# Kernel optimization log

Measured on AMD Instinct MI355X. Metric: run time of the kernel, lower is better.

The kernel has to match this reference:

```python
import jax, jax.numpy as jnp
import numpy as np


def _iterative_inv(mat, n_iter=6):
    # Newton-Schulz iteration for pseudo-inverse of [B,H,M,M] matrices
    I = jnp.eye(mat.shape[-1], dtype=mat.dtype)
    K = mat
    scale = 1.0 / jnp.max(jnp.sum(K, axis=-2), axis=-1)[..., None, None]
    V = scale * jnp.swapaxes(K, -1, -2)
    for _ in range(n_iter):
        KV = K @ V
        V = 0.25 * V @ (13.0 * I - KV @ (15.0 * I - KV @ (7.0 * I - KV)))
    return V


def setup_inputs() -> dict:
    key = jax.random.key(0)
    B, L, d_model, H, M = 4, 4096, 1024, 16, 128
    ks = jax.random.split(key, 11)
    s = 0.02
    return {
        "queries": jax.random.normal(ks[0], (B, L, d_model), jnp.float32),
        "keys": jax.random.normal(ks[1], (B, L, d_model), jnp.float32),
        "values": jax.random.normal(ks[2], (B, L, d_model), jnp.float32),
        "Wq": jax.random.normal(ks[3], (d_model, d_model), jnp.float32) * s,
        "bq": jnp.zeros((d_model,), jnp.float32),
        "Wk": jax.random.normal(ks[4], (d_model, d_model), jnp.float32) * s,
        "bk": jnp.zeros((d_model,), jnp.float32),
        "Wv": jax.random.normal(ks[5], (d_model, d_model), jnp.float32) * s,
        "bv": jnp.zeros((d_model,), jnp.float32),
        "Wo": jax.random.normal(ks[6], (d_model, d_model), jnp.float32) * s,
        "bo": jnp.zeros((d_model,), jnp.float32),
        "n_heads": 16,
        "n_landmarks": 128,
    }


def reference(queries, keys, values, Wq, bq, Wk, bk, Wv, bv, Wo, bo, n_heads, n_landmarks):
    B, L, _ = queries.shape
    H, M = n_heads, n_landmarks
    # projections -> [B, H, L, D]
    q = (queries @ Wq + bq).reshape(B, L, H, -1).transpose(0, 2, 1, 3)
    k = (keys @ Wk + bk).reshape(B, L, H, -1).transpose(0, 2, 1, 3)
    v = (values @ Wv + bv).reshape(B, L, H, -1).transpose(0, 2, 1, 3)
    D = q.shape[-1]
    # landmark pooling: mean over segments of length L//M
    Q_l = q.reshape(B, H, M, L // M, D).mean(axis=-2)
    K_l = k.reshape(B, H, M, L // M, D).mean(axis=-2)
    # three softmax kernels (NOTE: original has no 1/sqrt(D) scaling)
    kernel_1 = jax.nn.softmax(jnp.einsum('bhld,bhmd->bhlm', q, K_l), axis=-1)
    kernel_2 = jax.nn.softmax(jnp.einsum('bhnd,bhmd->bhnm', Q_l, K_l), axis=-1)
    kernel_3 = jax.nn.softmax(jnp.einsum('bhmd,bhld->bhml', Q_l, k), axis=-1)
    # [B,H,L,M] @ [B,H,M,M] @ ([B,H,M,L] @ [B,H,L,D])
    X = kernel_1 @ _iterative_inv(kernel_2) @ (kernel_3 @ v)
    X = X.transpose(0, 2, 1, 3).reshape(B, L, H * D)
    return X @ Wo + bo
```

## Files before the change

### kernel.cpp

```cpp
#include <hip/hip_runtime.h>

typedef __attribute__((ext_vector_type(8))) short s8v;
typedef __attribute__((ext_vector_type(4))) short s4v;
typedef __attribute__((ext_vector_type(4))) float f4v;

#define DEVI static __device__ __forceinline__

DEVI unsigned short f2bf(float f) {
  unsigned u = __float_as_uint(f);
  u = (u + 0x7FFFu + ((u >> 16) & 1u)) >> 16;
  return (unsigned short)u;
}
DEVI float bf2f(unsigned short b) { return __uint_as_float(((unsigned)b) << 16); }

#define MFMA(a, b, c) __builtin_amdgcn_mfma_f32_16x16x32_bf16((a), (b), (c), 0, 0, 0)

__global__ __launch_bounds__(256) void k_wt(const float* __restrict__ W,
                                            unsigned short* __restrict__ WT) {
  __shared__ unsigned short T[64][72];
  const int n0 = blockIdx.x * 64, k0 = blockIdx.y * 64;
  const int t = threadIdx.x;
  {
    const int r = t >> 2, c0 = (t & 3) * 16;
    const float* src = W + (k0 + r) * 1024 + n0 + c0;
#pragma unroll
    for (int jj = 0; jj < 4; ++jj) {
      f4v v = *(const f4v*)(src + jj * 4);
#pragma unroll
      for (int e = 0; e < 4; ++e) T[r][c0 + jj * 4 + e] = f2bf(v[e]);
    }
// ... 1 lines not shown
  __syncthreads();
  {
    const int n = t >> 2, c0 = (t & 3) * 16;
    unsigned short* dst = WT + (n0 + n) * 1024 + k0 + c0;
    s8v o0, o1;
#pragma unroll
    for (int j = 0; j < 8; ++j) {
      o0[j] = (short)T[c0 + j][n];
      o1[j] = (short)T[c0 + 8 + j][n];
    }
    *(s8v*)dst = o0;
    *(s8v*)(dst + 8) = o1;
  }
}

template <bool AF32, bool OF32>
__global__ __launch_bounds__(256, 2) void k_gemm(const void* __restrict__ Ap,
                                                 const unsigned short* __restrict__ Bt,
                                                 const float* __restrict__ bias,
                                                 void* __restrict__ Outp) {
  __shared__ unsigned short As[128 * 40];
  __shared__ unsigned short Bs[128 * 40];
  const int n0 = blockIdx.x * 128, m0 = blockIdx.y * 128;
  const int t = threadIdx.x, lane = t & 63, w = t >> 6;
  const int c16 = lane & 15, g = lane >> 4;
  const int wr = (w >> 1) * 64, wc = (w & 1) * 64;
  const int srow = t >> 1, skc = (t & 1) * 16;
  f4v acc[4][4] = {};
  for (int kt = 0; kt < 32; ++kt) {
    const int kb = kt * 32;
    s8v a0, a1, b0, b1;
    if (AF32) {
      const float* a = (const float*)Ap + (m0 + srow) * 1024 + kb + skc;
#pragma unroll
      for (int j = 0; j < 2; ++j) {
        f4v v0 = *(const f4v*)(a + j * 8);
        f4v v1 = *(const f4v*)(a + j * 8 + 4);
#pragma unroll
        for (int e = 0; e < 4; ++e) {
          if (j == 0) { a0[e] = (short)f2bf(v0[e]); a0[4 + e] = (short)f2bf(v1[e]); }
          else        { a1[e] = (short)f2bf(v0[e]); a1[4 + e] = (short)f2bf(v1[e]); }
        }
      }
    } else {
      const unsigned short* a = (const unsigned short*)Ap + (m0 + srow) * 1024 + kb + skc;
      a0 = *(const s8v*)a;
      a1 = *(const s8v*)(a + 8);
    }
    {
      const unsigned short* bsrc = Bt + (n0 + srow) * 1024 + kb + skc;
      b0 = *(const s8v*)bsrc;
      b1 = *(const s8v*)(bsrc + 8);
    }
    __syncthreads();
    *(s8v*)&As[srow * 40 + skc] = a0;
    *(s8v*)&As[srow * 40 + skc + 8] = a1;
    *(s8v*)&Bs[srow * 40 + skc] = b0;
    *(s8v*)&Bs[srow * 40 + skc + 8] = b1;
    __syncthreads();
    s8v afr[4], bfr[4];
#pragma unroll
    for (int mi = 0; mi < 4; ++mi) afr[mi] = *(s8v*)&As[(wr + mi * 16 + c16) * 40 + 8 * g];
#pragma unroll
    for (int ni = 0; ni < 4; ++ni) bfr[ni] = *(s8v*)&Bs[(wc + ni * 16 + c16) * 40 + 8 * g];
#pragma unroll
    for (int mi = 0; mi < 4; ++mi)
#pragma unroll
      for (int ni = 0; ni < 4; ++ni) acc[mi][ni] = MFMA(afr[mi], bfr[ni], acc[mi][ni]);
  }
  float bvv[4];
#pragma unroll
  for (int ni = 0; ni < 4; ++ni) bvv[ni] = bias[n0 + wc + ni * 16 + c16];
#pragma unroll
  for (int mi = 0; mi < 4; ++mi)
#pragma unroll
    for (int r = 0; r < 4; ++r) {
      const int row = m0 + wr + mi * 16 + 4 * g + r;
#pragma unroll
      for (int ni = 0; ni < 4; ++ni) {
        const int col = n0 + wc + ni * 16 + c16;
        const float v = acc[mi][ni][r] + bvv[ni];
        if (OF32) ((float*)Outp)[row * 1024 + col] = v;
        else ((unsigned short*)Outp)[row * 1024 + col] = f2bf(v);
      }
    }
}

__global__ __launch_bounds__(256) void k_land(const unsigned short* __restrict__ qb,
                                              const unsigned short* __restrict__ kb,
                                              float* __restrict__ Qlf, float* __restrict__ Klf,
                                              unsigned short* __restrict__ Qlb,
                                              unsigned short* __restrict__ Klb) {
// ... 3 lines not shown
  unsigned short* dB = which ? Klb : Qlb;
  const int m = blockIdx.x * 4 + (threadIdx.x >> 6);
  const int d = threadIdx.x & 63;
  const int b = bh >> 4, h = bh & 15;
  const unsigned short* p = src + ((b * 4096 + m * 32) * 16 + h) * 64 + d;
  float s = 0.f;
#pragma unroll 8
  for (int i = 0; i < 32; ++i) s += bf2f(p[i * 1024]);
  s *= (1.0f / 32.0f);
  dF[(bh * 128 + m) * 64 + d] = s;
  dB[(bh * 128 + m) * 64 + d] = f2bf(s);
}

__global__ __launch_bounds__(256) void k_k2(const float* __restrict__ Qlf,
                                            const float* __restrict__ Klf,
                                            float* __restrict__ K2, float* __restrict__ V0,
                                            float* __restrict__ V0T) {
  __shared__ float LS[8192];
  __shared__ float aux[132];
  unsigned short* P2 = (unsigned short*)LS;
  const int bh = blockIdx.x;
  const int t = threadIdx.x;
  const float* Kb = Klf + bh * 8192;
  for (int i = t; i < 8192; i += 256) LS[i] = Kb[i];
  __syncthreads();
  const int m = t >> 1, ch = t & 1;
  const float* Qr = Qlf + bh * 8192 + m * 64;
  float dv[64];
#pragma unroll
  for (int n = 0; n < 64; ++n) {
    const float* kr = &LS[(ch * 64 + n) * 64];
    float s = 0.f;
    for (int j = 0; j < 64; ++j) s = fmaf(Qr[j], kr[j], s);
    dv[n] = s;
  }
  float mx = -1e30f;
#pragma unroll
  for (int n = 0; n < 64; ++n) mx = fmaxf(mx, dv[n]);
  mx = fmaxf(mx, __shfl_xor(mx, 1));
  float sm = 0.f;
#pragma unroll
  for (int n = 0; n < 64; ++n) {
    dv[n] = __expf(dv[n] - mx);
    sm += dv[n];
  }
  sm += __shfl_xor(sm, 1);
  const float is = 1.0f / sm;
  float* K2r = K2 + bh * 16384 + m * 128 + ch * 64;
#pragma unroll
  for (int n = 0; n < 64; ++n) {
    dv[n] *= is;
    K2r[n] = dv[n];
  }
  __syncthreads();
#pragma unroll
  for (int n = 0; n < 64; ++n) P2[m * 128 + ch * 64 + n] = f2bf(dv[n]);
  __syncthreads();
  if (t < 128) {
    float s = 0.f;
    for (int i = 0; i < 128; ++i) s += bf2f(P2[i * 128 + t]);
    aux[t] = s;
  }
  __syncthreads();
  if (t < 64) {
    float v = fmaxf(aux[t], aux[t + 64]);
#pragma unroll
    for (int off = 1; off < 64; off <<= 1) v = fmaxf(v, __shfl_xor(v, off));
    if (t == 0) aux[128] = 1.0f / v;
  }
  __syncthreads();
  const float scale = aux[128];
  float* V0b = V0 + bh * 16384;
  float* V0Tb = V0T + bh * 16384;
  for (int idx = t; idx < 16384; idx += 256) {
    const int mm = idx >> 7, nn = idx & 127;
    const float v = bf2f(P2[idx]) * scale;
    V0Tb[idx] = v;
    V0b[nn * 128 + mm] = v;
  }
}

template <int EPI>
__global__ __launch_bounds__(256) void k_nsmm(const float* __restrict__ A,
                                              const float* __restrict__ Bt,
                                              float* __restrict__ C, float* __restrict__ Ct,
                                              const float alpha) {
  __shared__ unsigned short Ah[64 * 40], Al[64 * 40], Bh[64 * 40], Bl[64 * 40];
  const int bh = blockIdx.y;
  const int m0 = (blockIdx.x >> 1) * 64, n0 = (blockIdx.x & 1) * 64;
  const float* Ab = A + bh * 16384;
  const float* Bb = Bt + bh * 16384;
  const int t = threadIdx.x, lane = t & 63, w = t >> 6;
  const int c16 = lane & 15, g = lane >> 4;
  const int wr = (w >> 1) * 32, wc = (w & 1) * 32;
  const int srow = t >> 2, sc = (t & 3) * 8;
  f4v acc[2][2] = {};
  for (int kc = 0; kc < 4; ++kc) {
    const float* pa = Ab + (m0 + srow) * 128 + kc * 32 + sc;
    const float* pb = Bb + (n0 + srow) * 128 + kc * 32 + sc;
    s8v ah, al, bhv, blv;
#pragma unroll
    for (int j = 0; j < 8; ++j) {
      float va = pa[j];
      unsigned short hh = f2bf(va);
      ah[j] = (short)hh;
      al[j] = (short)f2bf(va - bf2f(hh));
      float vx = pb[j];
      hh = f2bf(vx);
      bhv[j] = (short)hh;
      blv[j] = (short)f2bf(vx - bf2f(hh));
    }
    __syncthreads();
    *(s8v*)&Ah[srow * 40 + sc] = ah;
    *(s8v*)&Al[srow * 40 + sc] = al;
    *(s8v*)&Bh[srow * 40 + sc] = bhv;
    *(s8v*)&Bl[srow * 40 + sc] = blv;
    __syncthreads();
    s8v fah[2], fal[2], fbh[2], fbl[2];
#pragma unroll
    for (int i = 0; i < 2; ++i) {
      fah[i] = *(s8v*)&Ah[(wr + i * 16 + c16) * 40 + 8 * g];
      fal[i] = *(s8v*)&Al[(wr + i * 16 + c16) * 40 + 8 * g];
      fbh[i] = *(s8v*)&Bh[(wc + i * 16 + c16) * 40 + 8 * g];
      fbl[i] = *(s8v*)&Bl[(wc + i * 16 + c16) * 40 + 8 * g];
    }
#pragma unroll
    for (int mi = 0; mi < 2; ++mi)
#pragma unroll
      for (int ni = 0; ni < 2; ++ni) {
        acc[mi][ni] = MFMA(fah[mi], fbh[ni], acc[mi][ni]);
        acc[mi][ni] = MFMA(fah[mi], fbl[ni], acc[mi][ni]);
        acc[mi][ni] = MFMA(fal[mi], fbh[ni], acc[mi][ni]);
      }
  }
#pragma unroll
  for (int mi = 0; mi < 2; ++mi)
#pragma unroll
    for (int ni = 0; ni < 2; ++ni) {
      const int rowb = m0 + wr + mi * 16 + 4 * g;
      const int col = n0 + wc + ni * 16 + c16;
      f4v v = acc[mi][ni];
      if (EPI == 2) v *= 0.25f;
      if (EPI != 1) {
#pragma unroll
        for (int r = 0; r < 4; ++r) C[bh * 16384 + (rowb + r) * 128 + col] = v[r];
      }
      f4v tv;
#pragma unroll
      for (int r = 0; r < 4; ++r) {
        if (EPI == 2) tv[r] = v[r];
        else tv[r] = ((rowb + r) == col ? alpha : 0.f) - v[r];
      }
      *(f4v*)&Ct[bh * 16384 + col * 128 + rowb] = tv;
    }
}

__global__ __launch_bounds__(256) void k_vt(const unsigned short* __restrict__ vb,
                                            unsigned short* __restrict__ vT) {
  __shared__ unsigned short T[64][72];
  const int lt = blockIdx.x, bh = blockIdx.y;
  const int b = bh >> 4, h = bh & 15;
  const int t = threadIdx.x;
  {
    const int r = t >> 2, c0 = (t & 3) * 16;
    const unsigned short* src = vb + ((b * 4096 + lt * 64 + r) * 16 + h) * 64 + c0;
    *(s8v*)&T[r][c0] = *(const s8v*)src;
    *(s8v*)&T[r][c0 + 8] = *(const s8v*)(src + 8);
  }
  __syncthreads();
  {
    const int d = t >> 2, c0 = (t & 3) * 16;
    unsigned short* dst = vT + (bh * 80 + d) * 4096 + lt * 64 + c0;
    s8v o0, o1;
#pragma unroll
    for (int j = 0; j < 8; ++j) {
      o0[j] = (short)T[c0 + j][d];
      o1[j] = (short)T[c0 + 8 + j][d];
    }
    *(s8v*)dst = o0;
    *(s8v*)(dst + 8) = o1;
  }
}

__global__ void k_ones(unsigned short* __restrict__ vT) {
  const int bh = blockIdx.y;
  const int i = blockIdx.x * 256 + threadIdx.x;
  vT[(bh * 80 + 64) * 4096 + i] = 0x3F80;
}

__global__ __launch_bounds__(256) void k_flash(const unsigned short* __restrict__ Qlb,
                                               const unsigned short* __restrict__ kb,
                                               const unsigned short* __restrict__ vT,
                                               float* __restrict__ Opart,
                                               float* __restrict__ dpart) {
  __shared__ unsigned short P3[128 * 72];
  const int chunk = blockIdx.x, bh = blockIdx.y;
  const int b = bh >> 4, h = bh & 15;
  const int t = threadIdx.x, lane = t & 63, w = t >> 6;
  const int c16 = lane & 15, g = lane >> 4;
  s8v aq[8][2];
#pragma unroll
  for (int mi = 0; mi < 8; ++mi)
// ... 16 lines not shown
      p[mi] = a;
    }
    __syncthreads();
#pragma unroll
    for (int mi = 0; mi < 8; ++mi)
#pragma unroll
      for (int r = 0; r < 4; ++r)
        P3[(mi * 16 + 4 * g + r) * 72 + 16 * w + c16] = f2bf(__expf(p[mi][r]));
    __syncthreads();
#pragma unroll
    for (int ks = 0; ks < 2; ++ks) {
      s8v ap0 = *(s8v*)&P3[(32 * w + c16) * 72 + ks * 32 + 8 * g];
      s8v ap1 = *(s8v*)&P3[(32 * w + 16 + c16) * 72 + ks * 32 + 8 * g];
#pragma unroll
      for (int ni = 0; ni < 5; ++ni) {
        s8v bv = *(const s8v*)&vT[(bh * 80 + ni * 16 + c16) * 4096 + l0 + ks * 32 + 8 * g];
        accO[0][ni] = MFMA(ap0, bv, accO[0][ni]);
        accO[1][ni] = MFMA(ap1, bv, accO[1][ni]);
      }
    }
  }
  const int obase = (bh * 4 + chunk) * 128 * 64;
#pragma unroll
  for (int mi2 = 0; mi2 < 2; ++mi2)
#pragma unroll
    for (int ni = 0; ni < 4; ++ni)
#pragma unroll
      for (int r = 0; r < 4; ++r)
        Opart[obase + (32 * w + mi2 * 16 + 4 * g + r) * 64 + ni * 16 + c16] = accO[mi2][ni][r];
  if (c16 == 0) {
#pragma unroll
    for (int mi2 = 0; mi2 < 2; ++mi2)
#pragma unroll
      for (int r = 0; r < 4; ++r)
        dpart[(bh * 4 + chunk) * 128 + 32 * w + mi2 * 16 + 4 * g + r] = accO[mi2][4][r];
  }
}

__global__ __launch_bounds__(256) void k_comb(const float* __restrict__ Opart,
                                              const float* __restrict__ dpart,
                                              unsigned short* __restrict__ k3h,
                                              unsigned short* __restrict__ k3l) {
  const int bh = blockIdx.x;
  const int t = threadIdx.x;
  for (int idx = t; idx < 8192; idx += 256) {
    const int m = idx >> 6, d = idx & 63;
    float s = 0.f, den = 0.f;
#pragma unroll
    for (int c = 0; c < 4; ++c) {
      s += Opart[((bh * 4 + c) * 128 + m) * 64 + d];
      den += dpart[(bh * 4 + c) * 128 + m];
    }
    const float v = s / den;
    const unsigned short hh = f2bf(v);
    k3h[(bh * 64 + d) * 128 + m] = hh;
    k3l[(bh * 64 + d) * 128 + m] = f2bf(v - bf2f(hh));
  }
}

__global__ __launch_bounds__(256) void k_zmm(const float* __restrict__ inv,
                                             const unsigned short* __restrict__ k3h,
                                             const unsigned short* __restrict__ k3l,
                                             unsigned short* __restrict__ ZTh,
                                             unsigned short* __restrict__ ZTl) {
  __shared__ unsigned short Ah[128 * 40], Al[128 * 40];
  const int bh = blockIdx.x;
  const int t = threadIdx.x, lane = t & 63, w = t >> 6;
  const int c16 = lane & 15, g = lane >> 4;
  const int wr = w * 32;
  const int srow = t >> 1, sc = (t & 1) * 16;
  f4v acc[2][4] = {};
  for (int kc = 0; kc < 4; ++kc) {
    const float* pa = inv + bh * 16384 + srow * 128 + kc * 32 + sc;
    s8v h0, lo0, h1, lo1;
#pragma unroll
    for (int j = 0; j < 8; ++j) {
      float va = pa[j];
      unsigned short hh = f2bf(va);
      h0[j] = (short)hh;
      lo0[j] = (short)f2bf(va - bf2f(hh));
      va = pa[8 + j];
      hh = f2bf(va);
      h1[j] = (short)hh;
      lo1[j] = (short)f2bf(va - bf2f(hh));
    }
    __syncthreads();
    *(s8v*)&Ah[srow * 40 + sc] = h0;
    *(s8v*)&Ah[srow * 40 + sc + 8] = h1;
    *(s8v*)&Al[srow * 40 + sc] = lo0;
    *(s8v*)&Al[srow * 40 + sc + 8] = lo1;
    __syncthreads();
    s8v fah[2], fal[2];
#pragma unroll
    for (int mi = 0; mi < 2; ++mi) {
      fah[mi] = *(s8v*)&Ah[(wr + mi * 16 + c16) * 40 + 8 * g];
      fal[mi] = *(s8v*)&Al[(wr + mi * 16 + c16) * 40 + 8 * g];
    }
#pragma unroll
    for (int ni = 0; ni < 4; ++ni) {
      s8v fbh = *(const s8v*)&k3h[(bh * 64 + ni * 16 + c16) * 128 + kc * 32 + 8 * g];
      s8v fbl = *(const s8v*)&k3l[(bh * 64 + ni * 16 + c16) * 128 + kc * 32 + 8 * g];
#pragma unroll
      for (int mi = 0; mi < 2; ++mi) {
        acc[mi][ni] = MFMA(fah[mi], fbh, acc[mi][ni]);
        acc[mi][ni] = MFMA(fah[mi], fbl, acc[mi][ni]);
        acc[mi][ni] = MFMA(fal[mi], fbh, acc[mi][ni]);
      }
    }
  }
#pragma unroll
  for (int mi = 0; mi < 2; ++mi)
#pragma unroll
    for (int ni = 0; ni < 4; ++ni) {
      const int rowb = wr + mi * 16 + 4 * g;
      const int col = ni * 16 + c16;
      s4v hv, lv;
#pragma unroll
      for (int r = 0; r < 4; ++r) {
        const float z = acc[mi][ni][r];
        const unsigned short hh = f2bf(z);
        hv[r] = (short)hh;
        lv[r] = (short)f2bf(z - bf2f(hh));
      }
      *(s4v*)&ZTh[(bh * 64 + col) * 128 + rowb] = hv;
      *(s4v*)&ZTl[(bh * 64 + col) * 128 + rowb] = lv;
    }
}

__global__ __launch_bounds__(256) void k_p1(const unsigned short* __restrict__ qb,
                                            const unsigned short* __restrict__ Klb,
                                            unsigned short* __restrict__ P1) {
  const int lt = blockIdx.x, bh = blockIdx.y;
  const int b = bh >> 4, h = bh & 15;
  const int t = threadIdx.x, lane = t & 63, w = t >> 6;
  const int c16 = lane & 15, g = lane >> 4;
  const int lrow = lt * 64 + 16 * w + c16;
  const unsigned short* qr = &qb[((b * 4096 + lrow) * 16 + h) * 64];
  s8v aq0 = *(const s8v*)&qr[8 * g];
  s8v aq1 = *(const s8v*)&qr[32 + 8 * g];
  f4v acc[8];
#pragma unroll
// ... 13 lines not shown
#pragma unroll
    for (int off = 1; off < 16; off <<= 1) mx = fmaxf(mx, __shfl_xor(mx, off));
    float sm = 0.f;
#pragma unroll
    for (int ni = 0; ni < 8; ++ni) {
      const float e = __expf(acc[ni][r] - mx);
      acc[ni][r] = e;
      sm += e;
    }
#pragma unroll
    for (int off = 1; off < 16; off <<= 1) sm += __shfl_xor(sm, off);
    const float is = 1.0f / sm;
    const int row = lt * 64 + 16 * w + 4 * g + r;
#pragma unroll
    for (int ni = 0; ni < 8; ++ni)
      P1[(bh * 4096 + row) * 128 + ni * 16 + c16] = f2bf(acc[ni][r] * is);
  }
}

__global__ __launch_bounds__(256) void k_xg(const unsigned short* __restrict__ P1,
                                            const unsigned short* __restrict__ ZTh,
                                            const unsigned short* __restrict__ ZTl,
                                            unsigned short* __restrict__ Xb) {
  const int lt = blockIdx.x, bh = blockIdx.y;
  const int b = bh >> 4, h = bh & 15;
  const int t = threadIdx.x, lane = t & 63, w = t >> 6;
  const int c16 = lane & 15, g = lane >> 4;
  const int wr = w * 32;
  f4v acc[2][4] = {};
  for (int kc = 0; kc < 4; ++kc) {
    s8v ap[2];
#pragma unroll
    for (int mi = 0; mi < 2; ++mi)
      ap[mi] = *(const s8v*)&P1[(bh * 4096 + lt * 128 + wr + mi * 16 + c16) * 128 + kc * 32 + 8 * g];
#pragma unroll
    for (int ni = 0; ni < 4; ++ni) {
      s8v zh = *(const s8v*)&ZTh[(bh * 64 + ni * 16 + c16) * 128 + kc * 32 + 8 * g];
      s8v zl = *(const s8v*)&ZTl[(bh * 64 + ni * 16 + c16) * 128 + kc * 32 + 8 * g];
#pragma unroll
      for (int mi = 0; mi < 2; ++mi) {
        acc[mi][ni] = MFMA(ap[mi], zh, acc[mi][ni]);
        acc[mi][ni] = MFMA(ap[mi], zl, acc[mi][ni]);
      }
    }
  }
#pragma unroll
  for (int mi = 0; mi < 2; ++mi)
#pragma unroll
    for (int ni = 0; ni < 4; ++ni)
#pragma unroll
      for (int r = 0; r < 4; ++r) {
        const int row = lt * 128 + wr + mi * 16 + 4 * g + r;
        Xb[(b * 4096 + row) * 1024 + h * 64 + ni * 16 + c16] = f2bf(acc[mi][ni][r]);
      }
}

extern "C" void kernel_launch(void* const* d_in, const int* in_sizes, int n_in,
                              void* d_out, int out_size, void* d_ws, size_t ws_size,
                              hipStream_t stream) {
  (void)in_sizes; (void)n_in; (void)out_size;
  const float* queries = (const float*)d_in[0];
  const float* keys = (const float*)d_in[1];
  const float* values = (const float*)d_in[2];
  const float* Wq = (const float*)d_in[3];
  const float* bq = (const float*)d_in[4];
  const float* Wk = (const float*)d_in[5];
  const float* bk = (const float*)d_in[6];
  const float* Wv = (const float*)d_in[7];
  const float* bv = (const float*)d_in[8];
  const float* Wo = (const float*)d_in[9];
  const float* bo = (const float*)d_in[10];
  char* ws = (char*)d_ws;
  if (ws_size < (size_t)197263360) return;

  unsigned short* qb = (unsigned short*)(ws + 0);
  unsigned short* kb = (unsigned short*)(ws + 33554432);
  unsigned short* vb = (unsigned short*)(ws + 67108864);
  unsigned short* vT = (unsigned short*)(ws + 100663296);
  unsigned short* WT = (unsigned short*)(ws + 142606336);
  float* Qlf = (float*)(ws + 144703488);
  float* Klf = (float*)(ws + 146800640);
  unsigned short* Qlb = (unsigned short*)(ws + 148897792);
  unsigned short* Klb = (unsigned short*)(ws + 149946368);
  float* K2 = (float*)(ws + 150994944);
  float* Va = (float*)(ws + 155189248);
  float* VaT = (float*)(ws + 159383552);
  float* Vb = (float*)(ws + 163577856);
  float* VbT = (float*)(ws + 167772160);
  float* KV = (float*)(ws + 171966464);
  float* W1 = (float*)(ws + 176160768);
  float* W2 = (float*)(ws + 180355072);
  float* Opart = (float*)(ws + 184549376);
  float* dpart = (float*)(ws + 192937984);
  unsigned short* k3h = (unsigned short*)(ws + 193069056);
  unsigned short* k3l = (unsigned short*)(ws + 194117632);
  unsigned short* ZTh = (unsigned short*)(ws + 195166208);
  unsigned short* ZTl = (unsigned short*)(ws + 196214784);
  unsigned short* Xb = qb;
  unsigned short* P1 = (unsigned short*)d_out;

  k_wt<<<dim3(16, 16), 256, 0, stream>>>(Wq, WT);
  k_gemm<true, false><<<dim3(8, 128), 256, 0, stream>>>(queries, WT, bq, qb);
  k_wt<<<dim3(16, 16), 256, 0, stream>>>(Wk, WT);
  k_gemm<true, false><<<dim3(8, 128), 256, 0, stream>>>(keys, WT, bk, kb);
  k_wt<<<dim3(16, 16), 256, 0, stream>>>(Wv, WT);
  k_gemm<true, false><<<dim3(8, 128), 256, 0, stream>>>(values, WT, bv, vb);
  k_land<<<dim3(32, 64, 2), 256, 0, stream>>>(qb, kb, Qlf, Klf, Qlb, Klb);
  k_k2<<<dim3(64), 256, 0, stream>>>(Qlf, Klf, K2, Va, VaT);
  float* vin = Va; float* vinT = VaT; float* vout = Vb; float* voutT = VbT;
  for (int it = 0; it < 6; ++it) {
    k_nsmm<0><<<dim3(4, 64), 256, 0, stream>>>(K2, vinT, KV, W1, 7.0f);
    k_nsmm<1><<<dim3(4, 64), 256, 0, stream>>>(KV, W1, W2, W2, 15.0f);
    k_nsmm<1><<<dim3(4, 64), 256, 0, stream>>>(KV, W2, W1, W1, 13.0f);
    k_nsmm<2><<<dim3(4, 64), 256, 0, stream>>>(vin, W1, vout, voutT, 0.0f);
    float* tp = vin; vin = vout; vout = tp;
    tp = vinT; vinT = voutT; voutT = tp;
  }
  k_vt<<<dim3(64, 64), 256, 0, stream>>>(vb, vT);
  k_ones<<<dim3(16, 64), 256, 0, stream>>>(vT);
  k_flash<<<dim3(4, 64), 256, 0, stream>>>(Qlb, kb, vT, Opart, dpart);
  k_comb<<<dim3(64), 256, 0, stream>>>(Opart, dpart, k3h, k3l);
  k_zmm<<<dim3(64), 256, 0, stream>>>(vin, k3h, k3l, ZTh, ZTl);
  k_p1<<<dim3(64, 64), 256, 0, stream>>>(qb, Klb, P1);
  k_xg<<<dim3(32, 64), 256, 0, stream>>>(P1, ZTh, ZTl, Xb);
  k_wt<<<dim3(16, 16), 256, 0, stream>>>(Wo, WT);
  k_gemm<false, true><<<dim3(8, 128), 256, 0, stream>>>(Xb, WT, bo, (float*)d_out);
}
```

Baseline: 941.6 us.

## Fuse Newton-Schulz loop into one kernel and use direct-to-LDS GEMM loads

```diff
diff --git a/kernel.cpp b/kernel.cpp
--- a/kernel.cpp
+++ b/kernel.cpp
@@ -14,6 +14,27 @@
 DEVI float bf2f(unsigned short b) { return __uint_as_float(((unsigned)b) << 16); }
 
 #define MFMA(a, b, c) __builtin_amdgcn_mfma_f32_16x16x32_bf16((a), (b), (c), 0, 0, 0)
+
+DEVI void gload16(const void* gsrc, void* ldst) {
+  __builtin_amdgcn_global_load_lds(
+      (const __attribute__((address_space(1))) unsigned int*)gsrc,
+      (__attribute__((address_space(3))) unsigned int*)ldst, 16, 0, 0);
+}
+
+__global__ __launch_bounds__(256) void k_cvt(const float* __restrict__ s,
+                                             unsigned short* __restrict__ d) {
+  const long i = (long)blockIdx.x * 256 + threadIdx.x;
+  const float* p = s + i * 8;
+  f4v v0 = *(const f4v*)p;
+  f4v v1 = *(const f4v*)(p + 4);
+  s8v o;
+#pragma unroll
+  for (int e = 0; e < 4; ++e) {
+    o[e] = (short)f2bf(v0[e]);
+    o[4 + e] = (short)f2bf(v1[e]);
+  }
+  *(s8v*)(d + i * 8) = o;
+}
 
 __global__ __launch_bounds__(256) void k_wt(const float* __restrict__ W,
                                             unsigned short* __restrict__ WT) {
@@ -45,55 +66,36 @@
   }
 }
 
-template <bool AF32, bool OF32>
-__global__ __launch_bounds__(256, 2) void k_gemm(const void* __restrict__ Ap,
-                                                 const unsigned short* __restrict__ Bt,
-                                                 const float* __restrict__ bias,
-                                                 void* __restrict__ Outp) {
-  __shared__ unsigned short As[128 * 40];
-  __shared__ unsigned short Bs[128 * 40];
-  const int n0 = blockIdx.x * 128, m0 = blockIdx.y * 128;
+template <bool OF32>
+__global__ __launch_bounds__(256) void k_gemm(const unsigned short* __restrict__ A,
+                                              const unsigned short* __restrict__ Bt,
+                                              const float* __restrict__ bias,
+                                              void* __restrict__ Outp) {
+  __shared__ unsigned short As[128 * 32];
+  __shared__ unsigned short Bs[128 * 32];
+  int bid = blockIdx.x;
+  bid = ((bid & 7) << 7) + (bid >> 3);
+  const int n0 = (bid & 7) * 128;
+  const int m0 = (bid >> 3) * 128;
   const int t = threadIdx.x, lane = t & 63, w = t >> 6;
   const int c16 = lane & 15, g = lane >> 4;
   const int wr = (w >> 1) * 64, wc = (w & 1) * 64;
-  const int srow = t >> 1, skc = (t & 1) * 16;
+  const unsigned short* Ag = A + (long)(m0 + (t >> 2)) * 1024 + (t & 3) * 8;
+  const unsigned short* Bg = Bt + (long)(n0 + (t >> 2)) * 1024 + (t & 3) * 8;
   f4v acc[4][4] = {};
   for (int kt = 0; kt < 32; ++kt) {
     const int kb = kt * 32;
-    s8v a0, a1, b0, b1;
-    if (AF32) {
-      const float* a = (const float*)Ap + (m0 + srow) * 1024 + kb + skc;
-#pragma unroll
-      for (int j = 0; j < 2; ++j) {
-        f4v v0 = *(const f4v*)(a + j * 8);
-        f4v v1 = *(const f4v*)(a + j * 8 + 4);
-#pragma unroll
-        for (int e = 0; e < 4; ++e) {
-          if (j == 0) { a0[e] = (short)f2bf(v0[e]); a0[4 + e] = (short)f2bf(v1[e]); }
-          else        { a1[e] = (short)f2bf(v0[e]); a1[4 + e] = (short)f2bf(v1[e]); }
-        }
-      }
-    } else {
-      const unsigned short* a = (const unsigned short*)Ap + (m0 + srow) * 1024 + kb + skc;
-      a0 = *(const s8v*)a;
-      a1 = *(const s8v*)(a + 8);
-    }
-    {
-      const unsigned short* bsrc = Bt + (n0 + srow) * 1024 + kb + skc;
-      b0 = *(const s8v*)bsrc;
-      b1 = *(const s8v*)(bsrc + 8);
-    }
     __syncthreads();
-    *(s8v*)&As[srow * 40 + skc] = a0;
-    *(s8v*)&As[srow * 40 + skc + 8] = a1;
-    *(s8v*)&Bs[srow * 40 + skc] = b0;
-    *(s8v*)&Bs[srow * 40 + skc + 8] = b1;
+    gload16(Ag + kb, (char*)As + w * 1024);
+    gload16(Ag + kb + 64 * 1024, (char*)As + 4096 + w * 1024);
+    gload16(Bg + kb, (char*)Bs + w * 1024);
+    gload16(Bg + kb + 64 * 1024, (char*)Bs + 4096 + w * 1024);
     __syncthreads();
     s8v afr[4], bfr[4];
 #pragma unroll
-    for (int mi = 0; mi < 4; ++mi) afr[mi] = *(s8v*)&As[(wr + mi * 16 + c16) * 40 + 8 * g];
-#pragma unroll
-    for (int ni = 0; ni < 4; ++ni) bfr[ni] = *(s8v*)&Bs[(wc + ni * 16 + c16) * 40 + 8 * g];
+    for (int mi = 0; mi < 4; ++mi) afr[mi] = *(s8v*)&As[(wr + mi * 16 + c16) * 32 + 8 * g];
+#pragma unroll
+    for (int ni = 0; ni < 4; ++ni) bfr[ni] = *(s8v*)&Bs[(wc + ni * 16 + c16) * 32 + 8 * g];
 #pragma unroll
     for (int mi = 0; mi < 4; ++mi)
 #pragma unroll
@@ -106,7 +108,7 @@
   for (int mi = 0; mi < 4; ++mi)
 #pragma unroll
     for (int r = 0; r < 4; ++r) {
-      const int row = m0 + wr + mi * 16 + 4 * g + r;
+      const long row = m0 + wr + mi * 16 + 4 * g + r;
 #pragma unroll
       for (int ni = 0; ni < 4; ++ni) {
         const int col = n0 + wc + ni * 16 + c16;
@@ -140,22 +142,27 @@
 
 __global__ __launch_bounds__(256) void k_k2(const float* __restrict__ Qlf,
                                             const float* __restrict__ Klf,
-                                            float* __restrict__ K2, float* __restrict__ V0,
-                                            float* __restrict__ V0T) {
-  __shared__ float LS[8192];
-  __shared__ float aux[132];
-  unsigned short* P2 = (unsigned short*)LS;
+                                            unsigned short* __restrict__ K2h,
+                                            unsigned short* __restrict__ K2l,
+                                            unsigned short* __restrict__ Vh,
+                                            unsigned short* __restrict__ Vl,
+                                            float* __restrict__ scale) {
+  __shared__ float S[16384];
+  __shared__ float cs[128];
+  __shared__ float sred;
   const int bh = blockIdx.x;
   const int t = threadIdx.x;
-  const float* Kb = Klf + bh * 8192;
-  for (int i = t; i < 8192; i += 256) LS[i] = Kb[i];
+  for (int i = t; i < 8192; i += 256) {
+    S[i] = Klf[bh * 8192 + i];
+    S[8192 + i] = Qlf[bh * 8192 + i];
+  }
   __syncthreads();
   const int m = t >> 1, ch = t & 1;
-  const float* Qr = Qlf + bh * 8192 + m * 64;
+  const float* Qr = &S[8192 + m * 64];
   float dv[64];
 #pragma unroll
   for (int n = 0; n < 64; ++n) {
-    const float* kr = &LS[(ch * 64 + n) * 64];
+    const float* kr = &S[(ch * 64 + n) * 64];
     float s = 0.f;
     for (int j = 0; j < 64; ++j) s = fmaf(Qr[j], kr[j], s);
     dv[n] = s;
@@ -172,113 +179,327 @@
   }
   sm += __shfl_xor(sm, 1);
   const float is = 1.0f / sm;
-  float* K2r = K2 + bh * 16384 + m * 128 + ch * 64;
-#pragma unroll
-  for (int n = 0; n < 64; ++n) {
-    dv[n] *= is;
-    K2r[n] = dv[n];
-  }
   __syncthreads();
-#pragma unroll
-  for (int n = 0; n < 64; ++n) P2[m * 128 + ch * 64 + n] = f2bf(dv[n]);
+  float* Srow = &S[m * 128 + ch * 64];
+#pragma unroll
+  for (int n = 0; n < 64; ++n) Srow[n] = dv[n] * is;
   __syncthreads();
-  if (t < 128) {
-    float s = 0.f;
-    for (int i = 0; i < 128; ++i) s += bf2f(P2[i * 128 + t]);
-    aux[t] = s;
+  {
+    const int col = t & 127, part = t >> 7;
+    float s_ = 0.f;
+    for (int r = part * 64; r < part * 64 + 64; ++r) s_ += S[r * 128 + col];
+    if (part == 0) cs[col] = s_;
+    __syncthreads();
+    if (part == 1) cs[col] += s_;
+    __syncthreads();
+  }
+  if (t < 64) {
+    float v = fmaxf(cs[t], cs[t + 64]);
+#pragma unroll
+    for (int off = 1; off < 64; off <<= 1) v = fmaxf(v, __shfl_xor(v, off));
+    if (t == 0) {
+      sred = 1.0f / v;
+      scale[bh] = 1.0f / v;
+    }
   }
   __syncthreads();
-  if (t < 64) {
-    float v = fmaxf(aux[t], aux[t + 64]);
-#pragma unroll
-    for (int off = 1; off < 64; off <<= 1) v = fmaxf(v, __shfl_xor(v, off));
-    if (t == 0) aux[128] = 1.0f / v;
-  }
-  __syncthreads();
-  const float scale = aux[128];
-  float* V0b = V0 + bh * 16384;
-  float* V0Tb = V0T + bh * 16384;
+  const float sc = sred;
+  const long base = (long)bh * 16384;
   for (int idx = t; idx < 16384; idx += 256) {
-    const int mm = idx >> 7, nn = idx & 127;
-    const float v = bf2f(P2[idx]) * scale;
-    V0Tb[idx] = v;
-    V0b[nn * 128 + mm] = v;
-  }
-}
-
-template <int EPI>
-__global__ __launch_bounds__(256) void k_nsmm(const float* __restrict__ A,
-                                              const float* __restrict__ Bt,
-                                              float* __restrict__ C, float* __restrict__ Ct,
-                                              const float alpha) {
-  __shared__ unsigned short Ah[64 * 40], Al[64 * 40], Bh[64 * 40], Bl[64 * 40];
-  const int bh = blockIdx.y;
-  const int m0 = (blockIdx.x >> 1) * 64, n0 = (blockIdx.x & 1) * 64;
-  const float* Ab = A + bh * 16384;
-  const float* Bb = Bt + bh * 16384;
+    const int r = idx >> 7, c = idx & 127;
+    const float v = S[idx];
+    unsigned short hh = f2bf(v);
+    K2h[base + idx] = hh;
+    K2l[base + idx] = f2bf(v - bf2f(hh));
+    const float v0 = sc * S[c * 128 + r];
+    hh = f2bf(v0);
+    Vh[base + idx] = hh;
+    Vl[base + idx] = f2bf(v0 - bf2f(hh));
+  }
+}
+
+__global__ __launch_bounds__(256) void k_ns(
+    const unsigned short* __restrict__ K2h, const unsigned short* __restrict__ K2l,
+    unsigned short* __restrict__ Vh, unsigned short* __restrict__ Vl,
+    const unsigned short* __restrict__ k3h, const unsigned short* __restrict__ k3l,
+    const float* __restrict__ scale,
+    unsigned short* __restrict__ ZTh, unsigned short* __restrict__ ZTl) {
+  __shared__ unsigned short BA[2][128][136];
+  __shared__ unsigned short BB[2][128][136];
+  const int bh = blockIdx.x;
   const int t = threadIdx.x, lane = t & 63, w = t >> 6;
   const int c16 = lane & 15, g = lane >> 4;
-  const int wr = (w >> 1) * 32, wc = (w & 1) * 32;
-  const int srow = t >> 2, sc = (t & 3) * 8;
-  f4v acc[2][2] = {};
-  for (int kc = 0; kc < 4; ++kc) {
-    const float* pa = Ab + (m0 + srow) * 128 + kc * 32 + sc;
-    const float* pb = Bb + (n0 + srow) * 128 + kc * 32 + sc;
-    s8v ah, al, bhv, blv;
-#pragma unroll
-    for (int j = 0; j < 8; ++j) {
-      float va = pa[j];
-      unsigned short hh = f2bf(va);
-      ah[j] = (short)hh;
-      al[j] = (short)f2bf(va - bf2f(hh));
-      float vx = pb[j];
-      hh = f2bf(vx);
-      bhv[j] = (short)hh;
-      blv[j] = (short)f2bf(vx - bf2f(hh));
-    }
-    __syncthreads();
-    *(s8v*)&Ah[srow * 40 + sc] = ah;
-    *(s8v*)&Al[srow * 40 + sc] = al;
-    *(s8v*)&Bh[srow * 40 + sc] = bhv;
-    *(s8v*)&Bl[srow * 40 + sc] = blv;
-    __syncthreads();
-    s8v fah[2], fal[2], fbh[2], fbl[2];
-#pragma unroll
-    for (int i = 0; i < 2; ++i) {
-      fah[i] = *(s8v*)&Ah[(wr + i * 16 + c16) * 40 + 8 * g];
-      fal[i] = *(s8v*)&Al[(wr + i * 16 + c16) * 40 + 8 * g];
-      fbh[i] = *(s8v*)&Bh[(wc + i * 16 + c16) * 40 + 8 * g];
-      fbl[i] = *(s8v*)&Bl[(wc + i * 16 + c16) * 40 + 8 * g];
-    }
-#pragma unroll
-    for (int mi = 0; mi < 2; ++mi)
+  const int wr = (w >> 1) * 64, wc = (w & 1) * 64;
+  const int pr = t >> 2, pc = (t & 3) * 8;
+  unsigned short* SA = &BA[0][0][0];
+  unsigned short* SB = &BB[0][0][0];
+  const float sc = scale[bh];
+  const long kbase = (long)bh * 16384;
+
+#pragma unroll 1
+  for (int it = 0; it < 6; ++it) {
+    {
+      f4v acc[4][4] = {};
+#pragma unroll 1
+      for (int kc = 0; kc < 4; ++kc) {
+        __syncthreads();
+        gload16(K2h + kbase + pr * 128 + kc * 32 + pc, (char*)SA + w * 1024);
+        gload16(K2h + kbase + (64 + pr) * 128 + kc * 32 + pc, (char*)SA + 4096 + w * 1024);
+        gload16(K2l + kbase + pr * 128 + kc * 32 + pc, (char*)SA + 8192 + w * 1024);
+        gload16(K2l + kbase + (64 + pr) * 128 + kc * 32 + pc, (char*)SA + 12288 + w * 1024);
+        __syncthreads();
+        s8v ah[4], al[4], bhv[4], blv[4];
+#pragma unroll
+        for (int mi = 0; mi < 4; ++mi) {
+          ah[mi] = *(s8v*)&SA[(wr + mi * 16 + c16) * 32 + 8 * g];
+          al[mi] = *(s8v*)&SA[4096 + (wr + mi * 16 + c16) * 32 + 8 * g];
+        }
+        if (it == 0) {
+#pragma unroll
+          for (int ni = 0; ni < 4; ++ni) {
+            bhv[ni] = *(s8v*)&SA[(wc + ni * 16 + c16) * 32 + 8 * g];
+            blv[ni] = *(s8v*)&SA[4096 + (wc + ni * 16 + c16) * 32 + 8 * g];
+          }
+        } else {
+#pragma unroll
+          for (int ni = 0; ni < 4; ++ni) {
+            bhv[ni] = *(s8v*)&BB[0][wc + ni * 16 + c16][kc * 32 + 8 * g];
+            blv[ni] = *(s8v*)&BB[1][wc + ni * 16 + c16][kc * 32 + 8 * g];
+          }
+        }
+#pragma unroll
+        for (int mi = 0; mi < 4; ++mi)
+#pragma unroll
+          for (int ni = 0; ni < 4; ++ni) {
+            acc[mi][ni] = MFMA(ah[mi], bhv[ni], acc[mi][ni]);
+            acc[mi][ni] = MFMA(ah[mi], blv[ni], acc[mi][ni]);
+            acc[mi][ni] = MFMA(al[mi], bhv[ni], acc[mi][ni]);
+          }
+      }
+      __syncthreads();
+#pragma unroll
+      for (int mi = 0; mi < 4; ++mi)
+#pragma unroll
+        for (int ni = 0; ni < 4; ++ni) {
+          const int rb = wr + mi * 16 + 4 * g;
+          const int cc = wc + ni * 16 + c16;
+          s4v th, tl;
+#pragma unroll
+          for (int r = 0; r < 4; ++r) {
+            float v = acc[mi][ni][r];
+            if (it == 0) v *= sc;
+            const unsigned short hh = f2bf(v);
+            BA[0][rb + r][cc] = hh;
+            BA[1][rb + r][cc] = f2bf(v - bf2f(hh));
+            const float tv = ((rb + r) == cc ? 7.0f : 0.0f) - v;
+            const unsigned short thh = f2bf(tv);
+            th[r] = (short)thh;
+            tl[r] = (short)f2bf(tv - bf2f(thh));
+          }
+          *(s4v*)&BB[0][cc][rb] = th;
+          *(s4v*)&BB[1][cc][rb] = tl;
+        }
+      __syncthreads();
+    }
+    {
+      f4v acc[4][4] = {};
+#pragma unroll 1
+      for (int kc = 0; kc < 4; ++kc) {
+        s8v ah[4], al[4], bhv[4], blv[4];
+#pragma unroll
+        for (int mi = 0; mi < 4; ++mi) {
+          ah[mi] = *(s8v*)&BA[0][wr + mi * 16 + c16][kc * 32 + 8 * g];
+          al[mi] = *(s8v*)&BA[1][wr + mi * 16 + c16][kc * 32 + 8 * g];
+        }
+#pragma unroll
+        for (int ni = 0; ni < 4; ++ni) {
+          bhv[ni] = *(s8v*)&BB[0][wc + ni * 16 + c16][kc * 32 + 8 * g];
+          blv[ni] = *(s8v*)&BB[1][wc + ni * 16 + c16][kc * 32 + 8 * g];
+        }
+#pragma unroll
+        for (int mi = 0; mi < 4; ++mi)
+#pragma unroll
+          for (int ni = 0; ni < 4; ++ni) {
+            acc[mi][ni] = MFMA(ah[mi], bhv[ni], acc[mi][ni]);
+            acc[mi][ni] = MFMA(ah[mi], blv[ni], acc[mi][ni]);
+            acc[mi][ni] = MFMA(al[mi], bhv[ni], acc[mi][ni]);
+          }
+      }
+      __syncthreads();
+#pragma unroll
+      for (int mi = 0; mi < 4; ++mi)
+#pragma unroll
+        for (int ni = 0; ni < 4; ++ni) {
+          const int rb = wr + mi * 16 + 4 * g;
+          const int cc = wc + ni * 16 + c16;
+          s4v th, tl;
+#pragma unroll
+          for (int r = 0; r < 4; ++r) {
+            const float tv = ((rb + r) == cc ? 15.0f : 0.0f) - acc[mi][ni][r];
+            const unsigned short thh = f2bf(tv);
+            th[r] = (short)thh;
+            tl[r] = (short)f2bf(tv - bf2f(thh));
+          }
+          *(s4v*)&BB[0][cc][rb] = th;
+          *(s4v*)&BB[1][cc][rb] = tl;
+        }
+      __syncthreads();
+    }
+    {
+      f4v acc[4][4] = {};
+#pragma unroll 1
+      for (int kc = 0; kc < 4; ++kc) {
+        s8v ah[4], al[4], bhv[4], blv[4];
+#pragma unroll
+        for (int mi = 0; mi < 4; ++mi) {
+          ah[mi] = *(s8v*)&BA[0][wr + mi * 16 + c16][kc * 32 + 8 * g];
+          al[mi] = *(s8v*)&BA[1][wr + mi * 16 + c16][kc * 32 + 8 * g];
+        }
+#pragma unroll
+        for (int ni = 0; ni < 4; ++ni) {
+          bhv[ni] = *(s8v*)&BB[0][wc + ni * 16 + c16][kc * 32 + 8 * g];
+          blv[ni] = *(s8v*)&BB[1][wc + ni * 16 + c16][kc * 32 + 8 * g];
+        }
+#pragma unroll
+        for (int mi = 0; mi < 4; ++mi)
+#pragma unroll
+          for (int ni = 0; ni < 4; ++ni) {
+            acc[mi][ni] = MFMA(ah[mi], bhv[ni], acc[mi][ni]);
+            acc[mi][ni] = MFMA(ah[mi], blv[ni], acc[mi][ni]);
+            acc[mi][ni] = MFMA(al[mi], bhv[ni], acc[mi][ni]);
+          }
+      }
+      __syncthreads();
+#pragma unroll
+      for (int mi = 0; mi < 4; ++mi)
+#pragma unroll
+        for (int ni = 0; ni < 4; ++ni) {
+          const int rb = wr + mi * 16 + 4 * g;
+          const int cc = wc + ni * 16 + c16;
+          s4v th, tl;
+#pragma unroll
+          for (int r = 0; r < 4; ++r) {
+            const float tv = ((rb + r) == cc ? 13.0f : 0.0f) - acc[mi][ni][r];
+            const unsigned short thh = f2bf(tv);
+            th[r] = (short)thh;
+            tl[r] = (short)f2bf(tv - bf2f(thh));
+          }
+          *(s4v*)&BA[0][cc][rb] = th;
+          *(s4v*)&BA[1][cc][rb] = tl;
+        }
+      __syncthreads();
+    }
+    {
+      f4v acc[4][4] = {};
+#pragma unroll 1
+      for (int kc = 0; kc < 4; ++kc) {
+        __syncthreads();
+        gload16(Vh + kbase + pr * 128 + kc * 32 + pc, (char*)SB + w * 1024);
+        gload16(Vh + kbase + (64 + pr) * 128 + kc * 32 + pc, (char*)SB + 4096 + w * 1024);
+        gload16(Vl + kbase + pr * 128 + kc * 32 + pc, (char*)SB + 8192 + w * 1024);
+        gload16(Vl + kbase + (64 + pr) * 128 + kc * 32 + pc, (char*)SB + 12288 + w * 1024);
+        __syncthreads();
+        s8v ah[4], al[4], bhv[4], blv[4];
+#pragma unroll
+        for (int mi = 0; mi < 4; ++mi) {
+          ah[mi] = *(s8v*)&SB[(wr + mi * 16 + c16) * 32 + 8 * g];
+          al[mi] = *(s8v*)&SB[4096 + (wr + mi * 16 + c16) * 32 + 8 * g];
+        }
+#pragma unroll
+        for (int ni = 0; ni < 4; ++ni) {
+          bhv[ni] = *(s8v*)&BA[0][wc + ni * 16 + c16][kc * 32 + 8 * g];
+          blv[ni] = *(s8v*)&BA[1][wc + ni * 16 + c16][kc * 32 + 8 * g];
+        }
+#pragma unroll
+        for (int mi = 0; mi < 4; ++mi)
+#pragma unroll
+          for (int ni = 0; ni < 4; ++ni) {
+            acc[mi][ni] = MFMA(ah[mi], bhv[ni], acc[mi][ni]);
+            acc[mi][ni] = MFMA(ah[mi], blv[ni], acc[mi][ni]);
+            acc[mi][ni] = MFMA(al[mi], bhv[ni], acc[mi][ni]);
+          }
+      }
+      __syncthreads();
+#pragma unroll
+      for (int mi = 0; mi < 4; ++mi)
+#pragma unroll
+        for (int ni = 0; ni < 4; ++ni) {
+          const int rb = wr + mi * 16 + 4 * g;
+          const int cc = wc + ni * 16 + c16;
+          if (it < 5) {
+            s4v th, tl;
+#pragma unroll
+            for (int r = 0; r < 4; ++r) {
+              const float v = 0.25f * acc[mi][ni][r];
+              const unsigned short hh = f2bf(v);
+              const unsigned short ll = f2bf(v - bf2f(hh));
+              Vh[kbase + (rb + r) * 128 + cc] = hh;
+              Vl[kbase + (rb + r) * 128 + cc] = ll;
+              th[r] = (short)hh;
+              tl[r] = (short)ll;
+            }
+            *(s4v*)&BB[0][cc][rb] = th;
+            *(s4v*)&BB[1][cc][rb] = tl;
+          } else {
+#pragma unroll
+            for (int r = 0; r < 4; ++r) {
+              const float v = 0.25f * acc[mi][ni][r];
+              const unsigned short hh = f2bf(v);
+              BB[0][rb + r][cc] = hh;
+              BB[1][rb + r][cc] = f2bf(v - bf2f(hh));
+            }
+          }
+        }
+      __syncthreads();
+    }
+  }
+  {
+    f4v az[4][2] = {};
+    const int wcz = (w & 1) * 32;
+#pragma unroll 1
+    for (int kc = 0; kc < 4; ++kc) {
+      __syncthreads();
+      gload16(k3h + (long)bh * 8192 + pr * 128 + kc * 32 + pc, (char*)SA + w * 1024);
+      gload16(k3l + (long)bh * 8192 + pr * 128 + kc * 32 + pc, (char*)SA + 4096 + w * 1024);
+      __syncthreads();
+      s8v ah[4], al[4], bhv[2], blv[2];
+#pragma unroll
+      for (int mi = 0; mi < 4; ++mi) {
+        ah[mi] = *(s8v*)&BB[0][wr + mi * 16 + c16][kc * 32 + 8 * g];
+        al[mi] = *(s8v*)&BB[1][wr + mi * 16 + c16][kc * 32 + 8 * g];
+      }
 #pragma unroll
       for (int ni = 0; ni < 2; ++ni) {
-        acc[mi][ni] = MFMA(fah[mi], fbh[ni], acc[mi][ni]);
-        acc[mi][ni] = MFMA(fah[mi], fbl[ni], acc[mi][ni]);
-        acc[mi][ni] = MFMA(fal[mi], fbh[ni], acc[mi][ni]);
-      }
-  }
-#pragma unroll
-  for (int mi = 0; mi < 2; ++mi)
-#pragma unroll
-    for (int ni = 0; ni < 2; ++ni) {
-      const int rowb = m0 + wr + mi * 16 + 4 * g;
-      const int col = n0 + wc + ni * 16 + c16;
-      f4v v = acc[mi][ni];
-      if (EPI == 2) v *= 0.25f;
-      if (EPI != 1) {
-#pragma unroll
-        for (int r = 0; r < 4; ++r) C[bh * 16384 + (rowb + r) * 128 + col] = v[r];
-      }
-      f4v tv;
-#pragma unroll
-      for (int r = 0; r < 4; ++r) {
-        if (EPI == 2) tv[r] = v[r];
-        else tv[r] = ((rowb + r) == col ? alpha : 0.f) - v[r];
-      }
-      *(f4v*)&Ct[bh * 16384 + col * 128 + rowb] = tv;
-    }
+        bhv[ni] = *(s8v*)&SA[(wcz + ni * 16 + c16) * 32 + 8 * g];
+        blv[ni] = *(s8v*)&SA[2048 + (wcz + ni * 16 + c16) * 32 + 8 * g];
+      }
+#pragma unroll
+      for (int mi = 0; mi < 4; ++mi)
+#pragma unroll
+        for (int ni = 0; ni < 2; ++ni) {
+          az[mi][ni] = MFMA(ah[mi], bhv[ni], az[mi][ni]);
+          az[mi][ni] = MFMA(ah[mi], blv[ni], az[mi][ni]);
+          az[mi][ni] = MFMA(al[mi], bhv[ni], az[mi][ni]);
+        }
+    }
+#pragma unroll
+    for (int mi = 0; mi < 4; ++mi)
+#pragma unroll
+      for (int ni = 0; ni < 2; ++ni) {
+        const int rb = wr + mi * 16 + 4 * g;
+        const int cc = wcz + ni * 16 + c16;
+        s4v th, tl;
+#pragma unroll
+        for (int r = 0; r < 4; ++r) {
+          const float z = az[mi][ni][r];
+          const unsigned short hh = f2bf(z);
+          th[r] = (short)hh;
+          tl[r] = (short)f2bf(z - bf2f(hh));
+        }
+        *(s4v*)&ZTh[((long)bh * 64 + cc) * 128 + rb] = th;
+        *(s4v*)&ZTl[((long)bh * 64 + cc) * 128 + rb] = tl;
+      }
+  }
 }
 
 __global__ __launch_bounds__(256) void k_vt(const unsigned short* __restrict__ vb,
@@ -296,7 +517,7 @@
   __syncthreads();
   {
     const int d = t >> 2, c0 = (t & 3) * 16;
-    unsigned short* dst = vT + (bh * 80 + d) * 4096 + lt * 64 + c0;
+    unsigned short* dst = vT + ((long)bh * 80 + d) * 4096 + lt * 64 + c0;
     s8v o0, o1;
 #pragma unroll
     for (int j = 0; j < 8; ++j) {
@@ -306,12 +527,7 @@
     *(s8v*)dst = o0;
     *(s8v*)(dst + 8) = o1;
   }
-}
-
-__global__ void k_ones(unsigned short* __restrict__ vT) {
-  const int bh = blockIdx.y;
-  const int i = blockIdx.x * 256 + threadIdx.x;
-  vT[(bh * 80 + 64) * 4096 + i] = 0x3F80;
+  if (t < 64) vT[((long)bh * 80 + 64) * 4096 + lt * 64 + t] = 0x3F80;
 }
 
 __global__ __launch_bounds__(256) void k_flash(const unsigned short* __restrict__ Qlb,
@@ -358,13 +574,13 @@
       s8v ap1 = *(s8v*)&P3[(32 * w + 16 + c16) * 72 + ks * 32 + 8 * g];
 #pragma unroll
       for (int ni = 0; ni < 5; ++ni) {
-        s8v bv = *(const s8v*)&vT[(bh * 80 + ni * 16 + c16) * 4096 + l0 + ks * 32 + 8 * g];
+        s8v bv = *(const s8v*)&vT[((long)bh * 80 + ni * 16 + c16) * 4096 + l0 + ks * 32 + 8 * g];
         accO[0][ni] = MFMA(ap0, bv, accO[0][ni]);
         accO[1][ni] = MFMA(ap1, bv, accO[1][ni]);
       }
     }
   }
-  const int obase = (bh * 4 + chunk) * 128 * 64;
+  const long obase = ((long)bh * 4 + chunk) * 128 * 64;
 #pragma unroll
   for (int mi2 = 0; mi2 < 2; ++mi2)
 #pragma unroll
@@ -392,83 +608,14 @@
     float s = 0.f, den = 0.f;
 #pragma unroll
     for (int c = 0; c < 4; ++c) {
-      s += Opart[((bh * 4 + c) * 128 + m) * 64 + d];
+      s += Opart[(((long)bh * 4 + c) * 128 + m) * 64 + d];
       den += dpart[(bh * 4 + c) * 128 + m];
     }
     const float v = s / den;
     const unsigned short hh = f2bf(v);
-    k3h[(bh * 64 + d) * 128 + m] = hh;
-    k3l[(bh * 64 + d) * 128 + m] = f2bf(v - bf2f(hh));
-  }
-}
-
-__global__ __launch_bounds__(256) void k_zmm(const float* __restrict__ inv,
-                                             const unsigned short* __restrict__ k3h,
-                                             const unsigned short* __restrict__ k3l,
-                                             unsigned short* __restrict__ ZTh,
-                                             unsigned short* __restrict__ ZTl) {
-  __shared__ unsigned short Ah[128 * 40], Al[128 * 40];
-  const int bh = blockIdx.x;
-  const int t = threadIdx.x, lane = t & 63, w = t >> 6;
-  const int c16 = lane & 15, g = lane >> 4;
-  const int wr = w * 32;
-  const int srow = t >> 1, sc = (t & 1) * 16;
-  f4v acc[2][4] = {};
-  for (int kc = 0; kc < 4; ++kc) {
-    const float* pa = inv + bh * 16384 + srow * 128 + kc * 32 + sc;
-    s8v h0, lo0, h1, lo1;
-#pragma unroll
-    for (int j = 0; j < 8; ++j) {
-      float va = pa[j];
-      unsigned short hh = f2bf(va);
-      h0[j] = (short)hh;
-      lo0[j] = (short)f2bf(va - bf2f(hh));
-      va = pa[8 + j];
-      hh = f2bf(va);
-      h1[j] = (short)hh;
-      lo1[j] = (short)f2bf(va - bf2f(hh));
-    }
-    __syncthreads();
-    *(s8v*)&Ah[srow * 40 + sc] = h0;
-    *(s8v*)&Ah[srow * 40 + sc + 8] = h1;
-    *(s8v*)&Al[srow * 40 + sc] = lo0;
-    *(s8v*)&Al[srow * 40 + sc + 8] = lo1;
-    __syncthreads();
-    s8v fah[2], fal[2];
-#pragma unroll
-    for (int mi = 0; mi < 2; ++mi) {
-      fah[mi] = *(s8v*)&Ah[(wr + mi * 16 + c16) * 40 + 8 * g];
-      fal[mi] = *(s8v*)&Al[(wr + mi * 16 + c16) * 40 + 8 * g];
-    }
-#pragma unroll
-    for (int ni = 0; ni < 4; ++ni) {
-      s8v fbh = *(const s8v*)&k3h[(bh * 64 + ni * 16 + c16) * 128 + kc * 32 + 8 * g];
-      s8v fbl = *(const s8v*)&k3l[(bh * 64 + ni * 16 + c16) * 128 + kc * 32 + 8 * g];
-#pragma unroll
-      for (int mi = 0; mi < 2; ++mi) {
-        acc[mi][ni] = MFMA(fah[mi], fbh, acc[mi][ni]);
-        acc[mi][ni] = MFMA(fah[mi], fbl, acc[mi][ni]);
-        acc[mi][ni] = MFMA(fal[mi], fbh, acc[mi][ni]);
-      }
-    }
-  }
-#pragma unroll
-  for (int mi = 0; mi < 2; ++mi)
-#pragma unroll
-    for (int ni = 0; ni < 4; ++ni) {
-      const int rowb = wr + mi * 16 + 4 * g;
-      const int col = ni * 16 + c16;
-      s4v hv, lv;
-#pragma unroll
-      for (int r = 0; r < 4; ++r) {
-        const float z = acc[mi][ni][r];
-        const unsigned short hh = f2bf(z);
-        hv[r] = (short)hh;
-        lv[r] = (short)f2bf(z - bf2f(hh));
-      }
-      *(s4v*)&ZTh[(bh * 64 + col) * 128 + rowb] = hv;
-      *(s4v*)&ZTl[(bh * 64 + col) * 128 + rowb] = lv;
-    }
+    k3h[((long)bh * 64 + d) * 128 + m] = hh;
+    k3l[((long)bh * 64 + d) * 128 + m] = f2bf(v - bf2f(hh));
+  }
 }
 
 __global__ __launch_bounds__(256) void k_p1(const unsigned short* __restrict__ qb,
@@ -512,7 +659,7 @@
     const int row = lt * 64 + 16 * w + 4 * g + r;
 #pragma unroll
     for (int ni = 0; ni < 8; ++ni)
-      P1[(bh * 4096 + row) * 128 + ni * 16 + c16] = f2bf(acc[ni][r] * is);
+      P1[((long)bh * 4096 + row) * 128 + ni * 16 + c16] = f2bf(acc[ni][r] * is);
   }
 }
 
@@ -530,11 +677,11 @@
     s8v ap[2];
 #pragma unroll
     for (int mi = 0; mi < 2; ++mi)
-      ap[mi] = *(const s8v*)&P1[(bh * 4096 + lt * 128 + wr + mi * 16 + c16) * 128 + kc * 32 + 8 * g];
+      ap[mi] = *(const s8v*)&P1[((long)bh * 4096 + lt * 128 + wr + mi * 16 + c16) * 128 + kc * 32 + 8 * g];
 #pragma unroll
     for (int ni = 0; ni < 4; ++ni) {
-      s8v zh = *(const s8v*)&ZTh[(bh * 64 + ni * 16 + c16) * 128 + kc * 32 + 8 * g];
-      s8v zl = *(const s8v*)&ZTl[(bh * 64 + ni * 16 + c16) * 128 + kc * 32 + 8 * g];
+      s8v zh = *(const s8v*)&ZTh[((long)bh * 64 + ni * 16 + c16) * 128 + kc * 32 + 8 * g];
+      s8v zl = *(const s8v*)&ZTl[((long)bh * 64 + ni * 16 + c16) * 128 + kc * 32 + 8 * g];
 #pragma unroll
       for (int mi = 0; mi < 2; ++mi) {
         acc[mi][ni] = MFMA(ap[mi], zh, acc[mi][ni]);
@@ -549,7 +696,7 @@
 #pragma unroll
       for (int r = 0; r < 4; ++r) {
         const int row = lt * 128 + wr + mi * 16 + 4 * g + r;
-        Xb[(b * 4096 + row) * 1024 + h * 64 + ni * 16 + c16] = f2bf(acc[mi][ni][r]);
+        Xb[((long)b * 4096 + row) * 1024 + h * 64 + ni * 16 + c16] = f2bf(acc[mi][ni][r]);
       }
 }
 
@@ -574,53 +721,44 @@
   unsigned short* qb = (unsigned short*)(ws + 0);
   unsigned short* kb = (unsigned short*)(ws + 33554432);
   unsigned short* vb = (unsigned short*)(ws + 67108864);
-  unsigned short* vT = (unsigned short*)(ws + 100663296);
-  unsigned short* WT = (unsigned short*)(ws + 142606336);
-  float* Qlf = (float*)(ws + 144703488);
-  float* Klf = (float*)(ws + 146800640);
-  unsigned short* Qlb = (unsigned short*)(ws + 148897792);
-  unsigned short* Klb = (unsigned short*)(ws + 149946368);
-  float* K2 = (float*)(ws + 150994944);
-  float* Va = (float*)(ws + 155189248);
-  float* VaT = (float*)(ws + 159383552);
-  float* Vb = (float*)(ws + 163577856);
-  float* VbT = (float*)(ws + 167772160);
-  float* KV = (float*)(ws + 171966464);
-  float* W1 = (float*)(ws + 176160768);
-  float* W2 = (float*)(ws + 180355072);
-  float* Opart = (float*)(ws + 184549376);
-  float* dpart = (float*)(ws + 192937984);
-  unsigned short* k3h = (unsigned short*)(ws + 193069056);
-  unsigned short* k3l = (unsigned short*)(ws + 194117632);
-  unsigned short* ZTh = (unsigned short*)(ws + 195166208);
-  unsigned short* ZTl = (unsigned short*)(ws + 196214784);
+  unsigned short* ti = (unsigned short*)(ws + 100663296);
+  float* Opart = (float*)(ws + 100663296);
+  float* dpart = (float*)(ws + 109051904);
+  unsigned short* WT = (unsigned short*)(ws + 134217728);
+  unsigned short* vT = (unsigned short*)(ws + 136314880);
+  float* Qlf = (float*)(ws + 178257920);
+  float* Klf = (float*)(ws + 180355072);
+  unsigned short* Qlb = (unsigned short*)(ws + 182452224);
+  unsigned short* Klb = (unsigned short*)(ws + 183500800);
+  unsigned short* K2h = (unsigned short*)(ws + 184549376);
+  unsigned short* K2l = (unsigned short*)(ws + 186646528);
+  unsigned short* Vh = (unsigned short*)(ws + 188743680);
+  unsigned short* Vl = (unsigned short*)(ws + 190840832);
+  unsigned short* k3h = (unsigned short*)(ws + 192937984);
+  unsigned short* k3l = (unsigned short*)(ws + 193986560);
+  unsigned short* ZTh = (unsigned short*)(ws + 195035136);
+  unsigned short* ZTl = (unsigned short*)(ws + 196083712);
+  float* scale = (float*)(ws + 197132288);
   unsigned short* Xb = qb;
   unsigned short* P1 = (unsigned short*)d_out;
 
   k_wt<<<dim3(16, 16), 256, 0, stream>>>(Wq, WT);
-  k_gemm<true, false><<<dim3(8, 128), 256, 0, stream>>>(queries, WT, bq, qb);
+  k_cvt<<<dim3(8192), 256, 0, stream>>>(queries, ti);
+  k_gemm<false><<<dim3(1024), 256, 0, stream>>>(ti, WT, bq, qb);
   k_wt<<<dim3(16, 16), 256, 0, stream>>>(Wk, WT);
-  k_gemm<true, false><<<dim3(8, 128), 256, 0, stream>>>(keys, WT, bk, kb);
+  k_cvt<<<dim3(8192), 256, 0, stream>>>(keys, ti);
+  k_gemm<false><<<dim3(1024), 256, 0, stream>>>(ti, WT, bk, kb);
   k_wt<<<dim3(16, 16), 256, 0, stream>>>(Wv, WT);
-  k_gemm<true, false><<<dim3(8, 128), 256, 0, stream>>>(values, WT, bv, vb);
+  k_cvt<<<dim3(8192), 256, 0, stream>>>(values, ti);
+  k_gemm<false><<<dim3(1024), 256, 0, stream>>>(ti, WT, bv, vb);
   k_land<<<dim3(32, 64, 2), 256, 0, stream>>>(qb, kb, Qlf, Klf, Qlb, Klb);
-  k_k2<<<dim3(64), 256, 0, stream>>>(Qlf, Klf, K2, Va, VaT);
-  float* vin = Va; float* vinT = VaT; float* vout = Vb; float* voutT = VbT;
-  for (int it = 0; it < 6; ++it) {
-    k_nsmm<0><<<dim3(4, 64), 256, 0, stream>>>(K2, vinT, KV, W1, 7.0f);
-    k_nsmm<1><<<dim3(4, 64), 256, 0, stream>>>(KV, W1, W2, W2, 15.0f);
-    k_nsmm<1><<<dim3(4, 64), 256, 0, stream>>>(KV, W2, W1, W1, 13.0f);
-    k_nsmm<2><<<dim3(4, 64), 256, 0, stream>>>(vin, W1, vout, voutT, 0.0f);
-    float* tp = vin; vin = vout; vout = tp;
-    tp = vinT; vinT = voutT; voutT = tp;
-  }
+  k_k2<<<dim3(64), 256, 0, stream>>>(Qlf, Klf, K2h, K2l, Vh, Vl, scale);
   k_vt<<<dim3(64, 64), 256, 0, stream>>>(vb, vT);
-  k_ones<<<dim3(16, 64), 256, 0, stream>>>(vT);
   k_flash<<<dim3(4, 64), 256, 0, stream>>>(Qlb, kb, vT, Opart, dpart);
   k_comb<<<dim3(64), 256, 0, stream>>>(Opart, dpart, k3h, k3l);
-  k_zmm<<<dim3(64), 256, 0, stream>>>(vin, k3h, k3l, ZTh, ZTl);
+  k_ns<<<dim3(64), 256, 0, stream>>>(K2h, K2l, Vh, Vl, k3h, k3l, scale, ZTh, ZTl);
   k_p1<<<dim3(64, 64), 256, 0, stream>>>(qb, Klb, P1);
   k_xg<<<dim3(32, 64), 256, 0, stream>>>(P1, ZTh, ZTl, Xb);
   k_wt<<<dim3(16, 16), 256, 0, stream>>>(Wo, WT);
-  k_gemm<false, true><<<dim3(8, 128), 256, 0, stream>>>(Xb, WT, bo, (float*)d_out);
-}
+  k_gemm<true><<<dim3(1024), 256, 0, stream>>>(Xb, WT, bo, (float*)d_out);
+}
```

Result: faster. 789.8 us (-16.1%).
